# Kernel tuning notes

Hardware: AMD Instinct MI355X
Metric: run time of the kernel (lower is better)

The kernel has to match this reference:

```python
import jax, jax.numpy as jnp
import numpy as np
import math

B, S, D, H = 4, 2048, 1024, 16
DH = D // H  # head dim = 64


def setup_inputs() -> dict:
    key = jax.random.key(0)
    ks = jax.random.split(key, 6)
    x = jax.random.normal(ks[0], (B, S, D), dtype=jnp.float32)
    mask = jax.random.randint(ks[1], (B, 1, S, S), 0, 2, dtype=jnp.int32)
    # torch nn.Linear default init scale ~ 1/sqrt(fan_in); use small scale for stability
    w_qkv = jax.random.normal(ks[2], (D, 3 * D), dtype=jnp.float32) * (1.0 / math.sqrt(D))
    b_qkv = jax.random.normal(ks[3], (3 * D,), dtype=jnp.float32) * 0.01
    w_out = jax.random.normal(ks[4], (D, D), dtype=jnp.float32) * (1.0 / math.sqrt(D))
    b_out = jax.random.normal(ks[5], (D,), dtype=jnp.float32) * 0.01
    return {"x": x, "mask": mask, "w_qkv": w_qkv, "b_qkv": b_qkv, "w_out": w_out, "b_out": b_out}


def reference(x, mask, w_qkv, b_qkv, w_out, b_out):
    # Fused QKV projection: [B,S,3D]
    qkv = x @ w_qkv + b_qkv
    q, k, v = qkv[..., :D], qkv[..., D:2 * D], qkv[..., 2 * D:]
    # split heads -> [B,H,S,DH]
    def split(t):
        return t.reshape(B, S, H, DH).transpose(0, 2, 1, 3)
    q, k, v = split(q), split(k), split(v)
    # scores: [B,H,S,S]
    scores = jnp.einsum("bhqd,bhkd->bhqk", q, k) / jnp.sqrt(jnp.float32(DH))
    scores = jnp.where(mask == 0, jnp.float32(-1000.0), scores)
    attn = jax.nn.softmax(scores, axis=-1)
    ctx = jnp.einsum("bhqk,bhkd->bhqd", attn, v)  # [B,H,S,DH]
    ctx = ctx.transpose(0, 2, 1, 3).reshape(B, S, D)
    return ctx @ w_out + b_out
```

## Files before the change

### kernel.cpp

```cpp
#include <hip/hip_runtime.h>
#include <hip/hip_bf16.h>
#include <stdint.h>

#define B_  4
#define S_  2048
#define D_  1024
#define H_  16
#define DH_ 64
#define N3_ 3072

typedef __attribute__((ext_vector_type(8))) short  short8;
typedef __attribute__((ext_vector_type(8))) unsigned short ushort8;
typedef __attribute__((ext_vector_type(4))) float  float4v;

__device__ __forceinline__ float bf2f(unsigned short u) {
    union { unsigned int i; float f; } c; c.i = ((unsigned int)u) << 16; return c.f;
}
__device__ __forceinline__ unsigned short f2bf(float f) {
    union { float f; unsigned int i; } c; c.f = f;
    unsigned int x = c.i;
    return (unsigned short)((x + 0x7FFFu + ((x >> 16) & 1u)) >> 16);
}
__device__ __forceinline__ unsigned short f2bf_hu(float f) {
    union { float f; unsigned int i; } c; c.f = f;
    return (unsigned short)((c.i + 0x8000u) >> 16);
}

__global__ __launch_bounds__(256) void convert_x(
    const float* __restrict__ in, unsigned short* __restrict__ out, int n8)
{
    int g = blockIdx.x * 256 + threadIdx.x;
    if (g >= n8) return;
    const float4* p = (const float4*)(in + (size_t)g * 8);
    float4 a = p[0], b = p[1];
    ushort8 o;
    o[0] = f2bf(a.x); o[1] = f2bf(a.y); o[2] = f2bf(a.z); o[3] = f2bf(a.w);
    o[4] = f2bf(b.x); o[5] = f2bf(b.y); o[6] = f2bf(b.z); o[7] = f2bf(b.w);
    *(ushort8*)(out + (size_t)g * 8) = o;
}

__global__ __launch_bounds__(256) void convert_wT(
    const float* __restrict__ w, unsigned short* __restrict__ wt, int K, int N)
{
    __shared__ float t[32][33];
    const int row = threadIdx.x >> 5;
    const int col = threadIdx.x & 31;
    const int n0 = blockIdx.x * 32;
    const int k0 = blockIdx.y * 32;
#pragma unroll
    for (int i = 0; i < 4; ++i)
        t[row + 8 * i][col] = w[(size_t)(k0 + row + 8 * i) * N + n0 + col];
    __syncthreads();
#pragma unroll
    for (int i = 0; i < 4; ++i)
        wt[(size_t)(n0 + row + 8 * i) * K + k0 + col] = f2bf(t[col][row + 8 * i]);
}

template <int MODE>
__global__ __launch_bounds__(256) void gemm_bt(
    const unsigned short* __restrict__ a, const unsigned short* __restrict__ bt,
    const float* __restrict__ bias,
    unsigned short* __restrict__ q, unsigned short* __restrict__ k,
    unsigned short* __restrict__ v, float* __restrict__ out,
    int K, int N)
{
    __shared__ unsigned short As[128][72];
    __shared__ unsigned short Bs[128][72];

    const int tid  = threadIdx.x;
    const int wave = tid >> 6;
    const int lane = tid & 63;
    const int col  = lane & 15;
    const int quad = lane >> 4;
    const int wm   = (wave & 1) * 64;
    const int wn   = (wave >> 1) * 64;

    const int m0 = blockIdx.y * 128;
    const int n0 = blockIdx.x * 128;

    float4v acc[4][4] = {};

    for (int kt = 0; kt < K; kt += 64) {
#pragma unroll
        for (int i = 0; i < 4; ++i) {
            int g = tid + i * 256;
            int r = g >> 3;
            int c8 = (g & 7) * 8;
            *(ushort8*)&As[r][c8] = *(const ushort8*)(a  + (size_t)(m0 + r) * K + kt + c8);
            *(ushort8*)&Bs[r][c8] = *(const ushort8*)(bt + (size_t)(n0 + r) * K + kt + c8);
        }
        __syncthreads();

#pragma unroll
        for (int ks = 0; ks < 64; ks += 32) {
            short8 af[4], bf[4];
#pragma unroll
            for (int mi = 0; mi < 4; ++mi)
                af[mi] = *(const short8*)&As[wm + mi * 16 + col][ks + quad * 8];
#pragma unroll
            for (int ni = 0; ni < 4; ++ni)
                bf[ni] = *(const short8*)&Bs[wn + ni * 16 + col][ks + quad * 8];
#pragma unroll
            for (int mi = 0; mi < 4; ++mi)
#pragma unroll
                for (int ni = 0; ni < 4; ++ni)
                    acc[mi][ni] = __builtin_amdgcn_mfma_f32_16x16x32_bf16(
                        af[mi], bf[ni], acc[mi][ni], 0, 0, 0);
        }
        __syncthreads();
    }

#pragma unroll
    for (int mi = 0; mi < 4; ++mi) {
#pragma unroll
        for (int ni = 0; ni < 4; ++ni) {
            int n = n0 + wn + ni * 16 + col;
            float bv = bias[n];
#pragma unroll
            for (int r = 0; r < 4; ++r) {
                int m = m0 + wm + mi * 16 + quad * 4 + r;
                float val = acc[mi][ni][r] + bv;
                if (MODE == 0) {
                    int which = n >> 10;
                    int h  = (n & 1023) >> 6;
                    int dh = n & 63;
                    int bb = m >> 11;
                    int s  = m & 2047;
                    size_t off;
                    if (which == 2)
                        off = (((size_t)bb * H_ + h) * DH_ + dh) * S_ + s;
                    else
                        off = (((size_t)bb * H_ + h) * S_ + s) * DH_ + dh;
                    unsigned short* dst = (which == 0) ? q : ((which == 1) ? k : v);
                    dst[off] = f2bf(val);
                } else {
                    out[(size_t)m * N + n] = val;
                }
            }
        }
    }
}

__global__ __launch_bounds__(256) void attn_mfma(
    const unsigned short* __restrict__ q, const unsigned short* __restrict__ k,
    const unsigned short* __restrict__ vT, const int* __restrict__ mask,
    unsigned short* __restrict__ ctx)
{
    __shared__ unsigned short Ks[64][72];
    __shared__ unsigned short Vt[64][72];
    __shared__ unsigned short Ps[4][16][72];

    const int tid  = threadIdx.x;
    const int wave = tid >> 6;
    const int lane = tid & 63;
    const int col  = lane & 15;
    const int quad = lane >> 4;

    const int h  = blockIdx.y;
    const int bb = blockIdx.z;
    const int q0 = blockIdx.x * 64 + wave * 16;
    const int kvbase = ((bb * H_ + h) * S_) * DH_;
    const int vtbase = ((bb * H_ + h) * DH_) * S_;

    const float SC = 0.18033688011112042f;
    const unsigned short* qrow = q + kvbase + (q0 + col) * DH_;
    ushort8 qr0 = *(const ushort8*)(qrow + quad * 8);
    ushort8 qr1 = *(const ushort8*)(qrow + 32 + quad * 8);
    short8 qa0, qa1;
#pragma unroll
    for (int j = 0; j < 8; ++j) {
        qa0[j] = (short)f2bf(bf2f(qr0[j]) * SC);
        qa1[j] = (short)f2bf(bf2f(qr1[j]) * SC);
    }
    const float MASKED = -1442.6951f;

    const int* mptr[4];
#pragma unroll
    for (int r = 0; r < 4; ++r)
        mptr[r] = mask + (bb * S_ + q0 + quad * 4 + r) * S_ + col;

    float4v oacc[4] = {};
    float rsum[4] = {0.f, 0.f, 0.f, 0.f};

    for (int kt = 0; kt < S_ / 64; ++kt) {
        const int key0 = kt * 64;

#pragma unroll
        for (int i = 0; i < 2; ++i) {
            int g = tid + i * 256;
            int r  = g >> 3;
            int c8 = (g & 7) * 8;
            *(ushort8*)&Ks[r][c8] = *(const ushort8*)(k  + kvbase + (key0 + r) * DH_ + c8);
            *(ushort8*)&Vt[r][c8] = *(const ushort8*)(vT + vtbase + r * S_ + key0 + c8);
        }
        __syncthreads();

        float4v sc[4];
#pragma unroll
        for (int sub = 0; sub < 4; ++sub) {
            short8 b0 = *(const short8*)&Ks[sub * 16 + col][quad * 8];
            short8 b1 = *(const short8*)&Ks[sub * 16 + col][32 + quad * 8];
            float4v acs = {};
            acs = __builtin_amdgcn_mfma_f32_16x16x32_bf16(qa0, b0, acs, 0, 0, 0);
            acs = __builtin_amdgcn_mfma_f32_16x16x32_bf16(qa1, b1, acs, 0, 0, 0);
            sc[sub] = acs;
        }

#pragma unroll
        for (int sub = 0; sub < 4; ++sub)
#pragma unroll
        for (int r = 0; r < 4; ++r) {
            int mk = mptr[r][key0 + sub * 16];
            float s = (mk == 0) ? MASKED : sc[sub][r];
            float p = __builtin_amdgcn_exp2f(s);
            rsum[r] += p;
            Ps[wave][quad * 4 + r][sub * 16 + col] = f2bf_hu(p);
        }

        short8 pa0 = *(const short8*)&Ps[wave][col][quad * 8];
        short8 pa1 = *(const short8*)&Ps[wave][col][32 + quad * 8];
#pragma unroll
        for (int n = 0; n < 4; ++n) {
            short8 vb0 = *(const short8*)&Vt[n * 16 + col][quad * 8];
            short8 vb1 = *(const short8*)&Vt[n * 16 + col][32 + quad * 8];
            oacc[n] = __builtin_amdgcn_mfma_f32_16x16x32_bf16(pa0, vb0, oacc[n], 0, 0, 0);
            oacc[n] = __builtin_amdgcn_mfma_f32_16x16x32_bf16(pa1, vb1, oacc[n], 0, 0, 0);
        }
        __syncthreads();
    }

    float inv[4];
#pragma unroll
    for (int r = 0; r < 4; ++r) {
        float s = rsum[r];
#pragma unroll
        for (int msk = 1; msk < 16; msk <<= 1)
            s += __shfl_xor(s, msk);
        inv[r] = 1.0f / s;
    }
#pragma unroll
    for (int n = 0; n < 4; ++n)
#pragma unroll
    for (int r = 0; r < 4; ++r) {
        size_t off = ((size_t)bb * S_ + (q0 + quad * 4 + r)) * D_
                   + h * DH_ + n * 16 + col;
        ctx[off] = f2bf(oacc[n][r] * inv[r]);
    }
}

extern "C" void kernel_launch(void* const* d_in, const int* in_sizes, int n_in,
                              void* d_out, int out_size, void* d_ws, size_t ws_size,
                              hipStream_t stream)
{
    const float* x     = (const float*)d_in[0];
    const int*   mask  = (const int*)d_in[1];
    const float* w_qkv = (const float*)d_in[2];
    const float* b_qkv = (const float*)d_in[3];
    const float* w_out = (const float*)d_in[4];
    const float* b_out = (const float*)d_in[5];
    float* out = (float*)d_out;

    unsigned short* ws = (unsigned short*)d_ws;
    const size_t sz = (size_t)B_ * S_ * D_;
    unsigned short* q     = ws;
    unsigned short* kk    = ws + sz;
    unsigned short* v     = ws + 2 * sz;
    unsigned short* ctx   = ws + 3 * sz;
    unsigned short* xbf   = ws + 4 * sz;
    unsigned short* wqkvT = ws + 5 * sz;
    unsigned short* woutT = ws + 5 * sz + (size_t)N3_ * D_;

    convert_x<<<(int)(sz / (256 * 8)), 256, 0, stream>>>(x, xbf, (int)(sz / 8));
    convert_wT<<<dim3(N3_ / 32, D_ / 32), 256, 0, stream>>>(w_qkv, wqkvT, D_, N3_);
    convert_wT<<<dim3(D_ / 32, D_ / 32), 256, 0, stream>>>(w_out, woutT, D_, D_);

    gemm_bt<0><<<dim3(N3_ / 128, (B_ * S_) / 128), 256, 0, stream>>>(
        xbf, wqkvT, b_qkv, q, kk, v, nullptr, D_, N3_);

    attn_mfma<<<dim3(S_ / 64, H_, B_), 256, 0, stream>>>(q, kk, v, mask, ctx);

    gemm_bt<1><<<dim3(D_ / 128, (B_ * S_) / 128), 256, 0, stream>>>(
        ctx, woutT, b_out, nullptr, nullptr, nullptr, out, D_, D_);
}
```

Baseline: 415.5 us.

## Load GEMM and attention tiles via global_load_lds with XOR-swizzled LDS layout

Replaces the register-staged global-to-LDS copies in both the projection GEMM and the attention kernel with direct global_load_lds 16-byte transfers. The padded LDS rows become unpadded, and bank conflicts are avoided with an XOR swizzle of the 8-element column groups, applied consistently to the K, V and P tiles. The attention kernel also prefetches the mask values into registers before the tile load barrier. This removes VGPR round-trips and LDS store instructions, but depends on the swizzle mapping matching the global_load_lds lane layout exactly.

```diff
diff --git a/kernel.cpp b/kernel.cpp
--- a/kernel.cpp
+++ b/kernel.cpp
@@ -24,6 +24,12 @@
 __device__ __forceinline__ unsigned short f2bf_hu(float f) {
     union { float f; unsigned int i; } c; c.f = f;
     return (unsigned short)((c.i + 0x8000u) >> 16);
+}
+
+__device__ __forceinline__ void gll16(const void* g, void* l) {
+    __builtin_amdgcn_global_load_lds(
+        (const __attribute__((address_space(1))) unsigned int*)g,
+        (__attribute__((address_space(3))) unsigned int*)l, 16, 0, 0);
 }
 
 __global__ __launch_bounds__(256) void convert_x(
@@ -64,8 +70,8 @@
     unsigned short* __restrict__ v, float* __restrict__ out,
     int K, int N)
 {
-    __shared__ unsigned short As[128][72];
-    __shared__ unsigned short Bs[128][72];
+    __shared__ unsigned short As[128][64];
+    __shared__ unsigned short Bs[128][64];
 
     const int tid  = threadIdx.x;
     const int wave = tid >> 6;
@@ -78,28 +84,32 @@
     const int m0 = blockIdx.y * 128;
     const int n0 = blockIdx.x * 128;
 
+    const int srow0 = wave * 32 + (lane >> 3);
+    const int scg   = (lane & 7) ^ (lane >> 3);
+
     float4v acc[4][4] = {};
 
     for (int kt = 0; kt < K; kt += 64) {
 #pragma unroll
-        for (int i = 0; i < 4; ++i) {
-            int g = tid + i * 256;
-            int r = g >> 3;
-            int c8 = (g & 7) * 8;
-            *(ushort8*)&As[r][c8] = *(const ushort8*)(a  + (size_t)(m0 + r) * K + kt + c8);
-            *(ushort8*)&Bs[r][c8] = *(const ushort8*)(bt + (size_t)(n0 + r) * K + kt + c8);
+        for (int c = 0; c < 4; ++c) {
+            int row = srow0 + c * 8;
+            gll16(a  + (size_t)(m0 + row) * K + kt + scg * 8,
+                  (char*)As + wave * 4096 + c * 1024);
+            gll16(bt + (size_t)(n0 + row) * K + kt + scg * 8,
+                  (char*)Bs + wave * 4096 + c * 1024);
         }
         __syncthreads();
 
 #pragma unroll
         for (int ks = 0; ks < 64; ks += 32) {
+            const int sa = (((ks >> 3) + quad) ^ (col & 7)) * 8;
             short8 af[4], bf[4];
 #pragma unroll
             for (int mi = 0; mi < 4; ++mi)
-                af[mi] = *(const short8*)&As[wm + mi * 16 + col][ks + quad * 8];
+                af[mi] = *(const short8*)&As[wm + mi * 16 + col][sa];
 #pragma unroll
             for (int ni = 0; ni < 4; ++ni)
-                bf[ni] = *(const short8*)&Bs[wn + ni * 16 + col][ks + quad * 8];
+                bf[ni] = *(const short8*)&Bs[wn + ni * 16 + col][sa];
 #pragma unroll
             for (int mi = 0; mi < 4; ++mi)
 #pragma unroll
@@ -146,9 +156,9 @@
     const unsigned short* __restrict__ vT, const int* __restrict__ mask,
     unsigned short* __restrict__ ctx)
 {
-    __shared__ unsigned short Ks[64][72];
-    __shared__ unsigned short Vt[64][72];
-    __shared__ unsigned short Ps[4][16][72];
+    __shared__ unsigned short Ks[64][64];
+    __shared__ unsigned short Vt[64][64];
+    __shared__ unsigned short Ps[4][16][64];
 
     const int tid  = threadIdx.x;
     const int wave = tid >> 6;
@@ -179,27 +189,42 @@
     for (int r = 0; r < 4; ++r)
         mptr[r] = mask + (bb * S_ + q0 + quad * 4 + r) * S_ + col;
 
+    const int sw2   = wave & 1;
+    const int srow0 = sw2 * 32 + (lane >> 3);
+    const int scg   = (lane & 7) ^ (lane >> 3);
+    const int sw0   = (quad ^ (col & 7)) * 8;
+    const int sw1   = ((4 + quad) ^ (col & 7)) * 8;
+
     float4v oacc[4] = {};
     float rsum[4] = {0.f, 0.f, 0.f, 0.f};
 
     for (int kt = 0; kt < S_ / 64; ++kt) {
         const int key0 = kt * 64;
 
-#pragma unroll
-        for (int i = 0; i < 2; ++i) {
-            int g = tid + i * 256;
-            int r  = g >> 3;
-            int c8 = (g & 7) * 8;
-            *(ushort8*)&Ks[r][c8] = *(const ushort8*)(k  + kvbase + (key0 + r) * DH_ + c8);
-            *(ushort8*)&Vt[r][c8] = *(const ushort8*)(vT + vtbase + r * S_ + key0 + c8);
+        int mk[4][4];
+#pragma unroll
+        for (int sub = 0; sub < 4; ++sub)
+#pragma unroll
+            for (int r = 0; r < 4; ++r)
+                mk[sub][r] = mptr[r][key0 + sub * 16];
+
+#pragma unroll
+        for (int c = 0; c < 4; ++c) {
+            int r = srow0 + c * 8;
+            if (wave < 2)
+                gll16(k + kvbase + (key0 + r) * DH_ + scg * 8,
+                      (char*)Ks + sw2 * 4096 + c * 1024);
+            else
+                gll16(vT + vtbase + r * S_ + key0 + scg * 8,
+                      (char*)Vt + sw2 * 4096 + c * 1024);
         }
         __syncthreads();
 
         float4v sc[4];
 #pragma unroll
         for (int sub = 0; sub < 4; ++sub) {
-            short8 b0 = *(const short8*)&Ks[sub * 16 + col][quad * 8];
-            short8 b1 = *(const short8*)&Ks[sub * 16 + col][32 + quad * 8];
+            short8 b0 = *(const short8*)&Ks[sub * 16 + col][sw0];
+            short8 b1 = *(const short8*)&Ks[sub * 16 + col][sw1];
             float4v acs = {};
             acs = __builtin_amdgcn_mfma_f32_16x16x32_bf16(qa0, b0, acs, 0, 0, 0);
             acs = __builtin_amdgcn_mfma_f32_16x16x32_bf16(qa1, b1, acs, 0, 0, 0);
@@ -210,19 +235,20 @@
         for (int sub = 0; sub < 4; ++sub)
 #pragma unroll
         for (int r = 0; r < 4; ++r) {
-            int mk = mptr[r][key0 + sub * 16];
-            float s = (mk == 0) ? MASKED : sc[sub][r];
+            float s = (mk[sub][r] == 0) ? MASKED : sc[sub][r];
             float p = __builtin_amdgcn_exp2f(s);
             rsum[r] += p;
-            Ps[wave][quad * 4 + r][sub * 16 + col] = f2bf_hu(p);
-        }
-
-        short8 pa0 = *(const short8*)&Ps[wave][col][quad * 8];
-        short8 pa1 = *(const short8*)&Ps[wave][col][32 + quad * 8];
+            int rowp = quad * 4 + r;
+            int sg = (sub * 2 + (col >> 3)) ^ (rowp & 7);
+            Ps[wave][rowp][sg * 8 + (col & 7)] = f2bf_hu(p);
+        }
+
+        short8 pa0 = *(const short8*)&Ps[wave][col][sw0];
+        short8 pa1 = *(const short8*)&Ps[wave][col][sw1];
 #pragma unroll
         for (int n = 0; n < 4; ++n) {
-            short8 vb0 = *(const short8*)&Vt[n * 16 + col][quad * 8];
-            short8 vb1 = *(const short8*)&Vt[n * 16 + col][32 + quad * 8];
+            short8 vb0 = *(const short8*)&Vt[n * 16 + col][sw0];
+            short8 vb1 = *(const short8*)&Vt[n * 16 + col][sw1];
             oacc[n] = __builtin_amdgcn_mfma_f32_16x16x32_bf16(pa0, vb0, oacc[n], 0, 0, 0);
             oacc[n] = __builtin_amdgcn_mfma_f32_16x16x32_bf16(pa1, vb1, oacc[n], 0, 0, 0);
         }
```

New measurement: 391.0 us. 5.9% less time.
